# Performance work log

Hardware: AMD Instinct MI355X
Metric: run time of the kernel (lower is better)

## Reference

```python
import jax, jax.numpy as jnp
import numpy as np

DIM = 256
H = 8
HD = DIM // H
FFN = 4 * DIM
SCALE = HD ** -0.5


def _layernorm(x, g, b):
    mu = jnp.mean(x, axis=-1, keepdims=True)
    var = jnp.var(x, axis=-1, keepdims=True)
    return (x - mu) * jax.lax.rsqrt(var + 1e-5) * g + b


def _mha(xq, xkv, p, prefix, bias=None):
    B, N, _ = xq.shape
    M = xkv.shape[1]
    q = (xq @ p[prefix + '_q_w'] + p[prefix + '_q_b']).reshape(B, N, H, HD).transpose(0, 2, 1, 3)
    k = (xkv @ p[prefix + '_k_w'] + p[prefix + '_k_b']).reshape(B, M, H, HD).transpose(0, 2, 1, 3)
    v = (xkv @ p[prefix + '_v_w'] + p[prefix + '_v_b']).reshape(B, M, H, HD).transpose(0, 2, 1, 3)
    attn = jnp.einsum('bhnd,bhmd->bhnm', q, k) * SCALE
    if bias is not None:
        attn = attn + bias
    attn = jax.nn.softmax(attn, axis=-1)
    out = jnp.einsum('bhnm,bhmd->bhnd', attn, v).transpose(0, 2, 1, 3).reshape(B, N, DIM)
    return out @ p[prefix + '_o_w'] + p[prefix + '_o_b']


def _ffn(x, p):
    h = jax.nn.gelu(x @ p['ffn_w1'] + p['ffn_b1'], approximate=False)
    return h @ p['ffn_w2'] + p['ffn_b2']


def setup_inputs() -> dict:
    key = jax.random.key(0)
    ks = iter(jax.random.split(key, 40))
    B, N = 4, 1024
    inp = {
        'src_feats': jax.random.normal(next(ks), (B, N, DIM), jnp.float32),
        'tgt_feats': jax.random.normal(next(ks), (B, N, DIM), jnp.float32),
        'src_geo_bias': jax.random.normal(next(ks), (B, H, N, N), jnp.float32),
        'tgt_geo_bias': jax.random.normal(next(ks), (B, H, N, N), jnp.float32),
    }
    s = 0.02
    for pre in ('sa', 'ca'):
        for nm in ('q', 'k', 'v', 'o'):
            inp[f'{pre}_{nm}_w'] = jax.random.normal(next(ks), (DIM, DIM), jnp.float32) * s
            inp[f'{pre}_{nm}_b'] = jnp.zeros((DIM,), jnp.float32)
    for nm in ('ln_sa', 'ln_ca', 'ln_ff'):
        inp[nm + '_g'] = jnp.ones((DIM,), jnp.float32)
        inp[nm + '_b'] = jnp.zeros((DIM,), jnp.float32)
    inp['ffn_w1'] = jax.random.normal(next(ks), (DIM, FFN), jnp.float32) * s
    inp['ffn_b1'] = jnp.zeros((FFN,), jnp.float32)
    inp['ffn_w2'] = jax.random.normal(next(ks), (FFN, DIM), jnp.float32) * s
    inp['ffn_b2'] = jnp.zeros((DIM,), jnp.float32)
    return inp


def reference(src_feats, tgt_feats, src_geo_bias, tgt_geo_bias,
              sa_q_w, sa_q_b, sa_k_w, sa_k_b, sa_v_w, sa_v_b, sa_o_w, sa_o_b,
              ca_q_w, ca_q_b, ca_k_w, ca_k_b, ca_v_w, ca_v_b, ca_o_w, ca_o_b,
              ln_sa_g, ln_sa_b, ln_ca_g, ln_ca_b, ln_ff_g, ln_ff_b,
              ffn_w1, ffn_b1, ffn_w2, ffn_b2):
    p = dict(sa_q_w=sa_q_w, sa_q_b=sa_q_b, sa_k_w=sa_k_w, sa_k_b=sa_k_b,
             sa_v_w=sa_v_w, sa_v_b=sa_v_b, sa_o_w=sa_o_w, sa_o_b=sa_o_b,
             ca_q_w=ca_q_w, ca_q_b=ca_q_b, ca_k_w=ca_k_w, ca_k_b=ca_k_b,
             ca_v_w=ca_v_w, ca_v_b=ca_v_b, ca_o_w=ca_o_w, ca_o_b=ca_o_b,
             ffn_w1=ffn_w1, ffn_b1=ffn_b1, ffn_w2=ffn_w2, ffn_b2=ffn_b2)
    # 1. geometric self-attention (pre-norm residual)
    src = src_feats + _mha(_layernorm(src_feats, ln_sa_g, ln_sa_b), _layernorm(src_feats, ln_sa_g, ln_sa_b), p, 'sa', src_geo_bias)
    tgt = tgt_feats + _mha(_layernorm(tgt_feats, ln_sa_g, ln_sa_b), _layernorm(tgt_feats, ln_sa_g, ln_sa_b), p, 'sa', tgt_geo_bias)
    # 2. cross-attention (both use post-self-attn normed feats)
    src_n = _layernorm(src, ln_ca_g, ln_ca_b)
    tgt_n = _layernorm(tgt, ln_ca_g, ln_ca_b)
    src = src + _mha(src_n, tgt_n, p, 'ca')
    tgt = tgt + _mha(tgt_n, src_n, p, 'ca')
    # 3. FFN
    src = src + _ffn(_layernorm(src, ln_ff_g, ln_ff_b), p)
    tgt = tgt + _ffn(_layernorm(tgt, ln_ff_g, ln_ff_b), p)
    return (src, tgt)
```

## Files before the change

### kernel.cpp

```cpp
#include <hip/hip_runtime.h>
#include <math.h>

#define DIM   256
#define NHEAD 8
#define HD    32
#define SEQ   1024
#define BATCH 4
#define ROWS  (BATCH * SEQ)
#define ROWS2 (2 * ROWS)
#define FFND  1024
#define QKVN  768
#define ATT_SCALE 0.17677669529663687f

typedef __attribute__((ext_vector_type(8))) short   bf16x8;
typedef __attribute__((ext_vector_type(4))) float   f32x4;

__device__ __forceinline__ unsigned short f2bf(float x) {
    unsigned u = __float_as_uint(x);
    unsigned r = (u + 0x7fffu + ((u >> 16) & 1u)) >> 16;
    return (unsigned short)r;
}

typedef const __attribute__((address_space(1))) unsigned int* glds_gp;
typedef __attribute__((address_space(3))) unsigned int*       glds_lp;
__device__ __forceinline__ void glds16(const void* g, void* l) {
    __builtin_amdgcn_global_load_lds((glds_gp)g, (glds_lp)l, 16, 0, 0);
}

__global__ __launch_bounds__(256) void ln_kernel(
        const float* __restrict__ x, const float* __restrict__ g,
        const float* __restrict__ b, unsigned short* __restrict__ y) {
    const int wid  = threadIdx.x >> 6;
    const int lane = threadIdx.x & 63;
    const int row  = blockIdx.x * 4 + wid;
    float4 xv = ((const float4*)(x + (size_t)row * DIM))[lane];
    float s = xv.x + xv.y + xv.z + xv.w;
    #pragma unroll
    for (int off = 32; off >= 1; off >>= 1) s += __shfl_xor(s, off, 64);
    const float mu = s * (1.0f / DIM);
    const float dx = xv.x - mu, dy = xv.y - mu, dz = xv.z - mu, dw = xv.w - mu;
    float sq = dx * dx + dy * dy + dz * dz + dw * dw;
    #pragma unroll
    for (int off = 32; off >= 1; off >>= 1) sq += __shfl_xor(sq, off, 64);
    const float rs = rsqrtf(sq * (1.0f / DIM) + 1e-5f);
    const float4 gv = ((const float4*)g)[lane];
    const float4 bv = ((const float4*)b)[lane];
    ushort4 o;
    o.x = f2bf(dx * rs * gv.x + bv.x);
    o.y = f2bf(dy * rs * gv.y + bv.y);
    o.z = f2bf(dz * rs * gv.z + bv.z);
    o.w = f2bf(dw * rs * gv.w + bv.w);
    ((ushort4*)(y + (size_t)row * DIM))[lane] = o;
}

__global__ __launch_bounds__(256) void ln2_kernel(
        const float* __restrict__ x0, const float* __restrict__ x1,
        const float* __restrict__ g, const float* __restrict__ b,
        unsigned short* __restrict__ y) {
    const int wid  = threadIdx.x >> 6;
    const int lane = threadIdx.x & 63;
    const int row  = blockIdx.x * 4 + wid;
    const float* x = (row < ROWS) ? (x0 + (size_t)row * DIM)
                                  : (x1 + (size_t)(row - ROWS) * DIM);
    float4 xv = ((const float4*)x)[lane];
    float s = xv.x + xv.y + xv.z + xv.w;
    #pragma unroll
    for (int off = 32; off >= 1; off >>= 1) s += __shfl_xor(s, off, 64);
    const float mu = s * (1.0f / DIM);
    const float dx = xv.x - mu, dy = xv.y - mu, dz = xv.z - mu, dw = xv.w - mu;
    float sq = dx * dx + dy * dy + dz * dz + dw * dw;
    #pragma unroll
    for (int off = 32; off >= 1; off >>= 1) sq += __shfl_xor(sq, off, 64);
    const float rs = rsqrtf(sq * (1.0f / DIM) + 1e-5f);
    const float4 gv = ((const float4*)g)[lane];
    const float4 bv = ((const float4*)b)[lane];
    ushort4 o;
    o.x = f2bf(dx * rs * gv.x + bv.x);
    o.y = f2bf(dy * rs * gv.y + bv.y);
    o.z = f2bf(dz * rs * gv.z + bv.z);
    o.w = f2bf(dw * rs * gv.w + bv.w);
    ((ushort4*)(y + (size_t)row * DIM))[lane] = o;
}

__global__ __launch_bounds__(256) void convert_weights(
        const float* __restrict__ sa_q_w, const float* __restrict__ sa_k_w,
        const float* __restrict__ sa_v_w, const float* __restrict__ ca_q_w,
        const float* __restrict__ ca_k_w, const float* __restrict__ ca_v_w,
        const float* __restrict__ sa_o_w, const float* __restrict__ ca_o_w,
        const float* __restrict__ ffn_w1, const float* __restrict__ ffn_w2,
        const float* __restrict__ sa_q_b, const float* __restrict__ sa_k_b,
        const float* __restrict__ sa_v_b, const float* __restrict__ ca_q_b,
        const float* __restrict__ ca_k_b, const float* __restrict__ ca_v_b,
        unsigned short* __restrict__ sa_qkv_wt, unsigned short* __restrict__ ca_qkv_wt,
        unsigned short* __restrict__ sa_o_wt,   unsigned short* __restrict__ ca_o_wt,
        unsigned short* __restrict__ ffn1_wt,   unsigned short* __restrict__ ffn2_wt,
        float* __restrict__ sa_qkv_bias, float* __restrict__ ca_qkv_bias) {
    int gid = blockIdx.x * 256 + threadIdx.x;
    if (gid < 196608) {
        int n = gid >> 8, k = gid & 255, nn = n & 255;
        const float* w = (n < 256) ? sa_q_w : (n < 512) ? sa_k_w : sa_v_w;
        sa_qkv_wt[gid] = f2bf(w[k * 256 + nn]);
        return;
    }
    gid -= 196608;
    if (gid < 196608) {
        int n = gid >> 8, k = gid & 255, nn = n & 255;
        const float* w = (n < 256) ? ca_q_w : (n < 512) ? ca_k_w : ca_v_w;
        ca_qkv_wt[gid] = f2bf(w[k * 256 + nn]);
        return;
    }
    gid -= 196608;
    if (gid < 65536) { int n = gid >> 8, k = gid & 255; sa_o_wt[gid] = f2bf(sa_o_w[k * 256 + n]); return; }
    gid -= 65536;
    if (gid < 65536) { int n = gid >> 8, k = gid & 255; ca_o_wt[gid] = f2bf(ca_o_w[k * 256 + n]); return; }
    gid -= 65536;
    if (gid < 262144) { int n = gid >> 8,  k = gid & 255;  ffn1_wt[gid] = f2bf(ffn_w1[k * 1024 + n]); return; }
    gid -= 262144;
    if (gid < 262144) { int n = gid >> 10, k = gid & 1023; ffn2_wt[gid] = f2bf(ffn_w2[k * 256 + n]);  return; }
    gid -= 262144;
    if (gid < 768) {
        sa_qkv_bias[gid] = (gid < 256) ? sa_q_b[gid] : (gid < 512) ? sa_k_b[gid - 256] : sa_v_b[gid - 512];
        return;
    }
    gid -= 768;
    if (gid < 768) {
        ca_qkv_bias[gid] = (gid < 256) ? ca_q_b[gid] : (gid < 512) ? ca_k_b[gid - 256] : ca_v_b[gid - 512];
    }
}

template <bool GELU, int MODE>
__global__ __launch_bounds__(256) void gemm_bf16(
        const unsigned short* __restrict__ A, const unsigned short* __restrict__ Wt,
        const float* __restrict__ bias,
        const float* __restrict__ res_lo, const float* __restrict__ res_hi,
        float* __restrict__ Cf, unsigned short* __restrict__ Cb,
        unsigned short* __restrict__ vt_g,
        int N, int K, int rsplit) {
    __shared__ unsigned short As[64 * 64];
    __shared__ unsigned short Ws[64 * 64];
    const int t = threadIdx.x;
    const int w = t >> 6, lane = t & 63, quad = lane >> 4, l16 = lane & 15;
    const int wm = w >> 1, wn = w & 1;
    const int m0 = blockIdx.y * 64, n0 = blockIdx.x * 64;
    const int srow = lane >> 3;
    const int schunk = (lane & 7) ^ srow;

    f32x4 acc[2][2];
    #pragma unroll
    for (int i = 0; i < 2; i++)
        #pragma unroll
        for (int j = 0; j < 2; j++)
            acc[i][j] = (f32x4){0.f, 0.f, 0.f, 0.f};

    for (int k0 = 0; k0 < K; k0 += 64) {
        #pragma unroll
        for (int q = 0; q < 2; q++) {
            const int r0 = w * 16 + q * 8;
            glds16(&A [(size_t)(m0 + r0 + srow) * K + k0 + schunk * 8], &As[r0 * 64]);
            glds16(&Wt[(size_t)(n0 + r0 + srow) * K + k0 + schunk * 8], &Ws[r0 * 64]);
        }
        __syncthreads();
        #pragma unroll
        for (int kc = 0; kc < 2; kc++) {
            bf16x8 af[2], bfr[2];
            #pragma unroll
            for (int i = 0; i < 2; i++) {
                const int ra = wm * 32 + i * 16 + l16;
                const int rb = wn * 32 + i * 16 + l16;
                af[i]  = *(const bf16x8*)&As[ra * 64 + (((kc * 4 + quad) ^ (l16 & 7)) * 8)];
                bfr[i] = *(const bf16x8*)&Ws[rb * 64 + (((kc * 4 + quad) ^ (l16 & 7)) * 8)];
            }
            #pragma unroll
            for (int i = 0; i < 2; i++)
                #pragma unroll
                for (int j = 0; j < 2; j++)
                    acc[i][j] = __builtin_amdgcn_mfma_f32_16x16x32_bf16(af[i], bfr[j], acc[i][j], 0, 0, 0);
        }
        __syncthreads();
    }

    const float* res = nullptr;
    if (MODE == 0 && res_lo)
        res = (m0 < rsplit) ? res_lo : (res_hi - (size_t)rsplit * N);

    #pragma unroll
    for (int i = 0; i < 2; i++) {
        #pragma unroll
        for (int j = 0; j < 2; j++) {
            const int n = n0 + wn * 32 + j * 16 + l16;
            const float bv = bias[n];
            #pragma unroll
            for (int r = 0; r < 4; r++) {
                const int m = m0 + wm * 32 + i * 16 + quad * 4 + r;
                float v = acc[i][j][r] + bv;
                if (GELU) v = 0.5f * v * (1.0f + erff(v * 0.70710678118654752f));
                if (MODE == 0) {
                    if (res) v += res[(size_t)m * N + n];
                    Cf[(size_t)m * N + n] = v;
                } else if (MODE == 1) {
                    Cb[(size_t)m * N + n] = f2bf(v);
                } else {
                    if (n0 < 512) {
                        Cb[(size_t)m * 512 + n] = f2bf(v);
                    } else {
                        const int nn = n - 512, h = nn >> 5, d = nn & 31;
                        const int side = m >> 12, bb = (m >> 10) & 3, seq = m & 1023;
                        vt_g[(size_t)(side * 32 + bb * 8 + h) * 32768 + d * 1024 + seq] = f2bf(v);
                    }
                }
            }
        }
    }
}

template <bool HAS_BIAS>
__global__ __launch_bounds__(256) void attn_mfma(
        const unsigned short* __restrict__ qk, const unsigned short* __restrict__ vt,
        const float* __restrict__ bias_src, const float* __restrict__ bias_tgt,
        unsigned short* __restrict__ AO, int cross) {
    extern __shared__ char smem[];
    unsigned short* Kss = (unsigned short*)smem;
    unsigned short* Vts = (unsigned short*)(smem + 4096);
    unsigned short* Pss = (unsigned short*)(smem + 8192);
    float*          Bls = (float*)(smem + 17408);

    const int t = threadIdx.x;
    const int w = t >> 6, lane = t & 63, quad = lane >> 4, l16 = lane & 15;
    const int bh = blockIdx.y;
    const int side = bh >> 5, b = (bh >> 3) & 3, h = bh & 7;
    const int q0 = blockIdx.x * 64;
    const int qbase  = side * ROWS + b * SEQ;
    const int kvside = cross ? (1 - side) : side;
    const int kvbase = kvside * ROWS + b * SEQ;
    const int bhv = kvside * 32 + b * 8 + h;

    const bf16x8 aq = *(const bf16x8*)&qk[(size_t)(qbase + q0 + w * 16 + l16) * 512 + h * HD + quad * 8];

    const float* brow = nullptr;
    if (HAS_BIAS)
        brow = (side ? bias_tgt : bias_src)
             + ((size_t)(b * NHEAD + h) * SEQ + q0 + w * 16) * SEQ;

    const int krow  = w * 16 + (lane >> 2);
    const int kslot = (lane & 3) ^ ((lane >> 2) & 3);
    const int vrow  = w * 8 + (lane >> 3);
    const int vslot = (lane & 7) ^ ((lane >> 3) & 7);
    const int b_r   = lane >> 4;
    const int b_c   = (lane & 15) * 4;

    float lsum[4] = {0.f, 0.f, 0.f, 0.f};
    f32x4 o0 = (f32x4){0.f, 0.f, 0.f, 0.f};
    f32x4 o1 = (f32x4){0.f, 0.f, 0.f, 0.f};

    if (HAS_BIAS) {
        #pragma unroll
        for (int q = 0; q < 4; q++)
            glds16(&brow[(size_t)(q * 4 + b_r) * SEQ + b_c],
                   &Bls[w * 1024 + q * 256]);
    }

    for (int kt = 0; kt < SEQ / 64; kt++) {
        __syncthreads();
        glds16(&qk[(size_t)(kvbase + kt * 64 + krow) * 512 + 256 + h * HD + kslot * 8],
               &Kss[w * 16 * 32]);
        glds16(&vt[(size_t)bhv * 32768 + (size_t)vrow * 1024 + kt * 64 + vslot * 8],
               &Vts[w * 8 * 64]);
        __syncthreads();
        if (HAS_BIAS && kt + 1 < SEQ / 64) {
            #pragma unroll
            for (int q = 0; q < 4; q++)
                glds16(&brow[(size_t)(q * 4 + b_r) * SEQ + (kt + 1) * 64 + b_c],
                       &Bls[((kt + 1) & 1) * 4096 + w * 1024 + q * 256]);
        }

        f32x4 s[4];
        #pragma unroll
        for (int st = 0; st < 4; st++) {
            const bf16x8 kf = *(const bf16x8*)&Kss[(st * 16 + l16) * 32 + ((quad ^ (l16 & 3)) * 8)];
            f32x4 z = (f32x4){0.f, 0.f, 0.f, 0.f};
            s[st] = __builtin_amdgcn_mfma_f32_16x16x32_bf16(aq, kf, z, 0, 0, 0);
        }

        const float* bb = HAS_BIAS ? &Bls[(kt & 1) * 4096 + w * 1024] : nullptr;
        #pragma unroll
        for (int st = 0; st < 4; st++) {
            #pragma unroll
            for (int r = 0; r < 4; r++) {
                float v = s[st][r] * ATT_SCALE;
                if (HAS_BIAS) v += bb[(quad * 4 + r) * 64 + st * 16 + l16];
                const float p = __expf(v);
                lsum[r] += p;
                Pss[(w * 16 + quad * 4 + r) * 72 + st * 16 + l16] = f2bf(p);
            }
        }

        #pragma unroll
        for (int c = 0; c < 2; c++) {
            const bf16x8 ap  = *(const bf16x8*)&Pss[(w * 16 + l16) * 72 + c * 32 + quad * 8];
            const int slot = (((c * 4 + quad) ^ (l16 & 7)) * 8);
            const bf16x8 bv0 = *(const bf16x8*)&Vts[l16 * 64 + slot];
            const bf16x8 bv1 = *(const bf16x8*)&Vts[(16 + l16) * 64 + slot];
            o0 = __builtin_amdgcn_mfma_f32_16x16x32_bf16(ap, bv0, o0, 0, 0, 0);
            o1 = __builtin_amdgcn_mfma_f32_16x16x32_bf16(ap, bv1, o1, 0, 0, 0);
        }
    }

    #pragma unroll
    for (int r = 0; r < 4; r++) {
        float l = lsum[r];
        #pragma unroll
        for (int off = 1; off < 16; off <<= 1) l += __shfl_xor(l, off, 64);
        const float inv = 1.0f / l;
        const size_t orow = (size_t)(qbase + q0 + w * 16 + quad * 4 + r) * DIM + h * HD;
        AO[orow + l16]      = f2bf(o0[r] * inv);
        AO[orow + 16 + l16] = f2bf(o1[r] * inv);
    }
}

extern "C" void kernel_launch(void* const* d_in, const int* in_sizes, int n_in,
                              void* d_out, int out_size, void* d_ws, size_t ws_size,
                              hipStream_t stream) {
    const float* src_feats    = (const float*)d_in[0];
    const float* tgt_feats    = (const float*)d_in[1];
    const float* src_geo_bias = (const float*)d_in[2];
    const float* tgt_geo_bias = (const float*)d_in[3];
    const float* sa_q_w = (const float*)d_in[4];
    const float* sa_q_b = (const float*)d_in[5];
    const float* sa_k_w = (const float*)d_in[6];
    const float* sa_k_b = (const float*)d_in[7];
    const float* sa_v_w = (const float*)d_in[8];
    const float* sa_v_b = (const float*)d_in[9];
    const float* sa_o_w = (const float*)d_in[10];
    const float* sa_o_b = (const float*)d_in[11];
    const float* ca_q_w = (const float*)d_in[12];
    const float* ca_q_b = (const float*)d_in[13];
    const float* ca_k_w = (const float*)d_in[14];
    const float* ca_k_b = (const float*)d_in[15];
    const float* ca_v_w = (const float*)d_in[16];
    const float* ca_v_b = (const float*)d_in[17];
    const float* ca_o_w = (const float*)d_in[18];
    const float* ca_o_b = (const float*)d_in[19];
    const float* ln_sa_g = (const float*)d_in[20];
    const float* ln_sa_b = (const float*)d_in[21];
    const float* ln_ca_g = (const float*)d_in[22];
    const float* ln_ca_b = (const float*)d_in[23];
    const float* ln_ff_g = (const float*)d_in[24];
    const float* ln_ff_b = (const float*)d_in[25];
    const float* ffn_w1  = (const float*)d_in[26];
    const float* ffn_b1  = (const float*)d_in[27];
    const float* ffn_w2  = (const float*)d_in[28];
    const float* ffn_b2  = (const float*)d_in[29];

    float* out = (float*)d_out;

    char* ws = (char*)d_ws;
    unsigned short* Xn = (unsigned short*)(ws);
    unsigned short* QK = (unsigned short*)(ws + (4  << 20));
    unsigned short* VT = (unsigned short*)(ws + (12 << 20));
    unsigned short* AO = (unsigned short*)(ws + (16 << 20));
    unsigned short* Hh = (unsigned short*)(ws + (4  << 20));
    char* wp = ws + (20 << 20);
    unsigned short* sa_qkv_wt = (unsigned short*)wp;  wp += 768 * 256 * 2;
    unsigned short* ca_qkv_wt = (unsigned short*)wp;  wp += 768 * 256 * 2;
    unsigned short* sa_o_wt   = (unsigned short*)wp;  wp += 256 * 256 * 2;
    unsigned short* ca_o_wt   = (unsigned short*)wp;  wp += 256 * 256 * 2;
    unsigned short* ffn1_wt   = (unsigned short*)wp;  wp += 1024 * 256 * 2;
    unsigned short* ffn2_wt   = (unsigned short*)wp;  wp += 256 * 1024 * 2;
    float* sa_qkv_bias = (float*)wp;  wp += 768 * 4;
    float* ca_qkv_bias = (float*)wp;  wp += 768 * 4;

    const dim3 blk(256);
    const dim3 attn_grid(SEQ / 64, 64);
    const int smem_sa = 17408 + 2 * 4096 * 4;
    const int smem_ca = 17408;

    convert_weights<<<dim3(4103), blk, 0, stream>>>(
        sa_q_w, sa_k_w, sa_v_w, ca_q_w, ca_k_w, ca_v_w, sa_o_w, ca_o_w,
        ffn_w1, ffn_w2, sa_q_b, sa_k_b, sa_v_b, ca_q_b, ca_k_b, ca_v_b,
        sa_qkv_wt, ca_qkv_wt, sa_o_wt, ca_o_wt, ffn1_wt, ffn2_wt,
        sa_qkv_bias, ca_qkv_bias);

    ln2_kernel<<<dim3(ROWS2 / 4), blk, 0, stream>>>(src_feats, tgt_feats, ln_sa_g, ln_sa_b, Xn);
    gemm_bf16<false, 2><<<dim3(QKVN / 64, ROWS2 / 64), blk, 0, stream>>>(
        Xn, sa_qkv_wt, sa_qkv_bias, nullptr, nullptr, nullptr, QK, VT, QKVN, DIM, ROWS);
    attn_mfma<true><<<attn_grid, blk, smem_sa, stream>>>(QK, VT, src_geo_bias, tgt_geo_bias, AO, 0);
    gemm_bf16<false, 0><<<dim3(DIM / 64, ROWS2 / 64), blk, 0, stream>>>(
        AO, sa_o_wt, sa_o_b, src_feats, tgt_feats, out, nullptr, nullptr, DIM, DIM, ROWS);

    ln_kernel<<<dim3(ROWS2 / 4), blk, 0, stream>>>(out, ln_ca_g, ln_ca_b, Xn);
    gemm_bf16<false, 2><<<dim3(QKVN / 64, ROWS2 / 64), blk, 0, stream>>>(
        Xn, ca_qkv_wt, ca_qkv_bias, nullptr, nullptr, nullptr, QK, VT, QKVN, DIM, ROWS);
    attn_mfma<false><<<attn_grid, blk, smem_ca, stream>>>(QK, VT, nullptr, nullptr, AO, 1);
    gemm_bf16<false, 0><<<dim3(DIM / 64, ROWS2 / 64), blk, 0, stream>>>(
        AO, ca_o_wt, ca_o_b, out, out + (size_t)ROWS * DIM, out, nullptr, nullptr, DIM, DIM, ROWS);

    ln_kernel<<<dim3(ROWS2 / 4), blk, 0, stream>>>(out, ln_ff_g, ln_ff_b, Xn);
    gemm_bf16<true, 1><<<dim3(FFND / 64, ROWS2 / 64), blk, 0, stream>>>(
        Xn, ffn1_wt, ffn_b1, nullptr, nullptr, nullptr, Hh, nullptr, FFND, DIM, ROWS);
    gemm_bf16<false, 0><<<dim3(DIM / 64, ROWS2 / 64), blk, 0, stream>>>(
        Hh, ffn2_wt, ffn_b2, out, out + (size_t)ROWS * DIM, out, nullptr, nullptr, DIM, FFND, ROWS);
}
```

Before: 488.5 us.

## Double-buffer K/V in attention, prefetch bias to registers, add 128-tile GEMM

The attention kernel now double-buffers the K and V tiles in shared memory, so the next tile is staged while the current one is computed. The geometric bias is prefetched straight into registers instead of going through LDS, which removes one sync per iteration and the large dynamic shared allocation. Separately, a new 128x128-tile GEMM with a stronger XOR swizzle replaces the 64-tile GEMM for the QKV and FFN1 projections, to get more data reuse per block. The risks are higher register pressure (32 bias floats plus 16 accumulators) and fewer blocks in the launch grid.

```diff
diff --git a/kernel.cpp b/kernel.cpp
--- a/kernel.cpp
+++ b/kernel.cpp
@@ -213,16 +213,86 @@
     }
 }
 
+template <bool GELU, int MODE>
+__global__ __launch_bounds__(256) void gemm128(
+        const unsigned short* __restrict__ A, const unsigned short* __restrict__ Wt,
+        const float* __restrict__ bias,
+        float* __restrict__ Cf, unsigned short* __restrict__ Cb,
+        unsigned short* __restrict__ vt_g,
+        int N, int K) {
+    __shared__ unsigned short As[128 * 32];
+    __shared__ unsigned short Ws[128 * 32];
+    const int t = threadIdx.x;
+    const int w = t >> 6, lane = t & 63, quad = lane >> 4, l16 = lane & 15;
+    const int wm = w >> 1, wn = w & 1;
+    const int m0 = blockIdx.y * 128, n0 = blockIdx.x * 128;
+    const int srow = lane >> 2;
+    const int sc   = lane & 3;
+    const int schunk = sc ^ (srow & 3) ^ ((srow >> 2) & 3);
+    const int rdswz = (quad ^ (l16 & 3) ^ ((l16 >> 2) & 3)) * 8;
+
+    f32x4 acc[4][4];
+    #pragma unroll
+    for (int i = 0; i < 4; i++)
+        #pragma unroll
+        for (int j = 0; j < 4; j++)
+            acc[i][j] = (f32x4){0.f, 0.f, 0.f, 0.f};
+
+    for (int k0 = 0; k0 < K; k0 += 32) {
+        glds16(&A [(size_t)(m0 + w * 32 + srow) * K + k0 + schunk * 8],      &As[(w * 32) * 32]);
+        glds16(&A [(size_t)(m0 + w * 32 + 16 + srow) * K + k0 + schunk * 8], &As[(w * 32 + 16) * 32]);
+        glds16(&Wt[(size_t)(n0 + w * 32 + srow) * K + k0 + schunk * 8],      &Ws[(w * 32) * 32]);
+        glds16(&Wt[(size_t)(n0 + w * 32 + 16 + srow) * K + k0 + schunk * 8], &Ws[(w * 32 + 16) * 32]);
+        __syncthreads();
+        bf16x8 af[4], bfr[4];
+        #pragma unroll
+        for (int i = 0; i < 4; i++) {
+            af[i]  = *(const bf16x8*)&As[(wm * 64 + i * 16 + l16) * 32 + rdswz];
+            bfr[i] = *(const bf16x8*)&Ws[(wn * 64 + i * 16 + l16) * 32 + rdswz];
+        }
+        #pragma unroll
+        for (int i = 0; i < 4; i++)
+            #pragma unroll
+            for (int j = 0; j < 4; j++)
+                acc[i][j] = __builtin_amdgcn_mfma_f32_16x16x32_bf16(af[i], bfr[j], acc[i][j], 0, 0, 0);
+        __syncthreads();
+    }
+
+    #pragma unroll
+    for (int i = 0; i < 4; i++) {
+        #pragma unroll
+        for (int j = 0; j < 4; j++) {
+            const int n = n0 + wn * 64 + j * 16 + l16;
+            const float bv = bias[n];
+            #pragma unroll
+            for (int r = 0; r < 4; r++) {
+                const int m = m0 + wm * 64 + i * 16 + quad * 4 + r;
+                float v = acc[i][j][r] + bv;
+                if (GELU) v = 0.5f * v * (1.0f + erff(v * 0.70710678118654752f));
+                if (MODE == 1) {
+                    Cb[(size_t)m * N + n] = f2bf(v);
+                } else {
+                    if (n < 512) {
+                        Cb[(size_t)m * 512 + n] = f2bf(v);
+                    } else {
+                        const int nn = n - 512, h = nn >> 5, d = nn & 31;
+                        const int side = m >> 12, bb = (m >> 10) & 3, seq = m & 1023;
+                        vt_g[(size_t)(side * 32 + bb * 8 + h) * 32768 + d * 1024 + seq] = f2bf(v);
+                    }
+                }
+            }
+        }
+    }
+}
+
 template <bool HAS_BIAS>
 __global__ __launch_bounds__(256) void attn_mfma(
         const unsigned short* __restrict__ qk, const unsigned short* __restrict__ vt,
         const float* __restrict__ bias_src, const float* __restrict__ bias_tgt,
         unsigned short* __restrict__ AO, int cross) {
-    extern __shared__ char smem[];
-    unsigned short* Kss = (unsigned short*)smem;
-    unsigned short* Vts = (unsigned short*)(smem + 4096);
-    unsigned short* Pss = (unsigned short*)(smem + 8192);
-    float*          Bls = (float*)(smem + 17408);
+    __shared__ unsigned short Kss[2 * 64 * 32];
+    __shared__ unsigned short Vts[2 * 32 * 64];
+    __shared__ unsigned short Pss[64 * 72];
 
     const int t = threadIdx.x;
     const int w = t >> 6, lane = t & 63, quad = lane >> 4, l16 = lane & 15;
@@ -241,53 +311,55 @@
         brow = (side ? bias_tgt : bias_src)
              + ((size_t)(b * NHEAD + h) * SEQ + q0 + w * 16) * SEQ;
 
-    const int krow  = w * 16 + (lane >> 2);
-    const int kslot = (lane & 3) ^ ((lane >> 2) & 3);
-    const int vrow  = w * 8 + (lane >> 3);
-    const int vslot = (lane & 7) ^ ((lane >> 3) & 7);
-    const int b_r   = lane >> 4;
-    const int b_c   = (lane & 15) * 4;
+    const int krow  = lane >> 2;
+    const int kslot = (lane & 3) ^ (krow & 3) ^ ((krow >> 2) & 3);
+    const int vrow  = lane >> 3;
+    const int vslot = (lane & 7) ^ (vrow & 7);
+    const int kswz  = (quad ^ (l16 & 3) ^ ((l16 >> 2) & 3)) * 8;
+
+    auto stageKV = [&](int kt, int bufi) {
+        glds16(&qk[(size_t)(kvbase + kt * 64 + w * 16 + krow) * 512 + 256 + h * HD + kslot * 8],
+               &Kss[bufi * 2048 + (w * 16) * 32]);
+        glds16(&vt[(size_t)bhv * 32768 + (size_t)(w * 8 + vrow) * 1024 + kt * 64 + vslot * 8],
+               &Vts[bufi * 2048 + (w * 8) * 64]);
+    };
 
     float lsum[4] = {0.f, 0.f, 0.f, 0.f};
     f32x4 o0 = (f32x4){0.f, 0.f, 0.f, 0.f};
     f32x4 o1 = (f32x4){0.f, 0.f, 0.f, 0.f};
-
-    if (HAS_BIAS) {
-        #pragma unroll
-        for (int q = 0; q < 4; q++)
-            glds16(&brow[(size_t)(q * 4 + b_r) * SEQ + b_c],
-                   &Bls[w * 1024 + q * 256]);
-    }
-
-    for (int kt = 0; kt < SEQ / 64; kt++) {
+    float breg0[16], breg1[16];
+
+    auto loadBias = [&](int kt, float (&d)[16]) {
+        #pragma unroll
+        for (int st = 0; st < 4; st++)
+            #pragma unroll
+            for (int r = 0; r < 4; r++)
+                d[st * 4 + r] = brow[(size_t)(quad * 4 + r) * SEQ + kt * 64 + st * 16 + l16];
+    };
+
+    stageKV(0, 0);
+    if (HAS_BIAS) loadBias(0, breg0);
+
+    auto iter = [&](int kt, float (&bcur)[16], float (&bnxt)[16]) {
+        const int cb = kt & 1;
         __syncthreads();
-        glds16(&qk[(size_t)(kvbase + kt * 64 + krow) * 512 + 256 + h * HD + kslot * 8],
-               &Kss[w * 16 * 32]);
-        glds16(&vt[(size_t)bhv * 32768 + (size_t)vrow * 1024 + kt * 64 + vslot * 8],
-               &Vts[w * 8 * 64]);
-        __syncthreads();
-        if (HAS_BIAS && kt + 1 < SEQ / 64) {
-            #pragma unroll
-            for (int q = 0; q < 4; q++)
-                glds16(&brow[(size_t)(q * 4 + b_r) * SEQ + (kt + 1) * 64 + b_c],
-                       &Bls[((kt + 1) & 1) * 4096 + w * 1024 + q * 256]);
-        }
+        if (kt < 15) stageKV(kt + 1, cb ^ 1);
 
         f32x4 s[4];
         #pragma unroll
         for (int st = 0; st < 4; st++) {
-            const bf16x8 kf = *(const bf16x8*)&Kss[(st * 16 + l16) * 32 + ((quad ^ (l16 & 3)) * 8)];
+            const bf16x8 kf = *(const bf16x8*)&Kss[cb * 2048 + (st * 16 + l16) * 32 + kswz];
             f32x4 z = (f32x4){0.f, 0.f, 0.f, 0.f};
             s[st] = __builtin_amdgcn_mfma_f32_16x16x32_bf16(aq, kf, z, 0, 0, 0);
         }
-
-        const float* bb = HAS_BIAS ? &Bls[(kt & 1) * 4096 + w * 1024] : nullptr;
+        if (HAS_BIAS && kt < 15) loadBias(kt + 1, bnxt);
+
         #pragma unroll
         for (int st = 0; st < 4; st++) {
             #pragma unroll
             for (int r = 0; r < 4; r++) {
                 float v = s[st][r] * ATT_SCALE;
-                if (HAS_BIAS) v += bb[(quad * 4 + r) * 64 + st * 16 + l16];
+                if (HAS_BIAS) v += bcur[st * 4 + r];
                 const float p = __expf(v);
                 lsum[r] += p;
                 Pss[(w * 16 + quad * 4 + r) * 72 + st * 16 + l16] = f2bf(p);
@@ -298,11 +370,16 @@
         for (int c = 0; c < 2; c++) {
             const bf16x8 ap  = *(const bf16x8*)&Pss[(w * 16 + l16) * 72 + c * 32 + quad * 8];
             const int slot = (((c * 4 + quad) ^ (l16 & 7)) * 8);
-            const bf16x8 bv0 = *(const bf16x8*)&Vts[l16 * 64 + slot];
-            const bf16x8 bv1 = *(const bf16x8*)&Vts[(16 + l16) * 64 + slot];
+            const bf16x8 bv0 = *(const bf16x8*)&Vts[cb * 2048 + l16 * 64 + slot];
+            const bf16x8 bv1 = *(const bf16x8*)&Vts[cb * 2048 + (16 + l16) * 64 + slot];
             o0 = __builtin_amdgcn_mfma_f32_16x16x32_bf16(ap, bv0, o0, 0, 0, 0);
             o1 = __builtin_amdgcn_mfma_f32_16x16x32_bf16(ap, bv1, o1, 0, 0, 0);
         }
+    };
+
+    for (int kt2 = 0; kt2 < 16; kt2 += 2) {
+        iter(kt2,     breg0, breg1);
+        iter(kt2 + 1, breg1, breg0);
     }
 
     #pragma unroll
@@ -371,8 +448,6 @@
 
     const dim3 blk(256);
     const dim3 attn_grid(SEQ / 64, 64);
-    const int smem_sa = 17408 + 2 * 4096 * 4;
-    const int smem_ca = 17408;
 
     convert_weights<<<dim3(4103), blk, 0, stream>>>(
         sa_q_w, sa_k_w, sa_v_w, ca_q_w, ca_k_w, ca_v_w, sa_o_w, ca_o_w,
@@ -381,22 +456,22 @@
         sa_qkv_bias, ca_qkv_bias);
 
     ln2_kernel<<<dim3(ROWS2 / 4), blk, 0, stream>>>(src_feats, tgt_feats, ln_sa_g, ln_sa_b, Xn);
-    gemm_bf16<false, 2><<<dim3(QKVN / 64, ROWS2 / 64), blk, 0, stream>>>(
-        Xn, sa_qkv_wt, sa_qkv_bias, nullptr, nullptr, nullptr, QK, VT, QKVN, DIM, ROWS);
-    attn_mfma<true><<<attn_grid, blk, smem_sa, stream>>>(QK, VT, src_geo_bias, tgt_geo_bias, AO, 0);
+    gemm128<false, 2><<<dim3(QKVN / 128, ROWS2 / 128), blk, 0, stream>>>(
+        Xn, sa_qkv_wt, sa_qkv_bias, nullptr, QK, VT, QKVN, DIM);
+    attn_mfma<true><<<attn_grid, blk, 0, stream>>>(QK, VT, src_geo_bias, tgt_geo_bias, AO, 0);
     gemm_bf16<false, 0><<<dim3(DIM / 64, ROWS2 / 64), blk, 0, stream>>>(
         AO, sa_o_wt, sa_o_b, src_feats, tgt_feats, out, nullptr, nullptr, DIM, DIM, ROWS);
 
     ln_kernel<<<dim3(ROWS2 / 4), blk, 0, stream>>>(out, ln_ca_g, ln_ca_b, Xn);
-    gemm_bf16<false, 2><<<dim3(QKVN / 64, ROWS2 / 64), blk, 0, stream>>>(
-        Xn, ca_qkv_wt, ca_qkv_bias, nullptr, nullptr, nullptr, QK, VT, QKVN, DIM, ROWS);
-    attn_mfma<false><<<attn_grid, blk, smem_ca, stream>>>(QK, VT, nullptr, nullptr, AO, 1);
+    gemm128<false, 2><<<dim3(QKVN / 128, ROWS2 / 128), blk, 0, stream>>>(
+        Xn, ca_qkv_wt, ca_qkv_bias, nullptr, QK, VT, QKVN, DIM);
+    attn_mfma<false><<<attn_grid, blk, 0, stream>>>(QK, VT, nullptr, nullptr, AO, 1);
     gemm_bf16<false, 0><<<dim3(DIM / 64, ROWS2 / 64), blk, 0, stream>>>(
         AO, ca_o_wt, ca_o_b, out, out + (size_t)ROWS * DIM, out, nullptr, nullptr, DIM, DIM, ROWS);
 
     ln_kernel<<<dim3(ROWS2 / 4), blk, 0, stream>>>(out, ln_ff_g, ln_ff_b, Xn);
-    gemm_bf16<true, 1><<<dim3(FFND / 64, ROWS2 / 64), blk, 0, stream>>>(
-        Xn, ffn1_wt, ffn_b1, nullptr, nullptr, nullptr, Hh, nullptr, FFND, DIM, ROWS);
+    gemm128<true, 1><<<dim3(FFND / 128, ROWS2 / 128), blk, 0, stream>>>(
+        Xn, ffn1_wt, ffn_b1, nullptr, Hh, nullptr, FFND, DIM);
     gemm_bf16<false, 0><<<dim3(DIM / 64, ROWS2 / 64), blk, 0, stream>>>(
         Hh, ffn2_wt, ffn_b2, out, out + (size_t)ROWS * DIM, out, nullptr, nullptr, DIM, FFND, ROWS);
 }
```

Result: slower. 504.0 us (+3.2%).
